# Kernel tuning notes

Hardware: AMD Instinct MI355X
Metric: run time of the kernel (lower is better)

Reference implementation:

```python
import jax, jax.numpy as jnp
import numpy as np

EMBED_DIM = 584  # module-global, used as softmax scale base (C ** -0.5)


def setup_inputs() -> dict:
    key = jax.random.key(0)
    ks = jax.random.split(key, 7)
    B, T, C, H, D = 16, 1024, 584, 8, 73
    x = jax.random.normal(ks[0], (B, T, C), dtype=jnp.float32)
    memory = jax.random.normal(ks[1], (B, T, C), dtype=jnp.float32)
    s = 0.02
    Wq = jax.random.normal(ks[2], (H, C, D), dtype=jnp.float32) * s
    Wk = jax.random.normal(ks[3], (H, C, D), dtype=jnp.float32) * s
    Wv = jax.random.normal(ks[4], (H, C, D), dtype=jnp.float32) * s
    Wp = jax.random.normal(ks[5], (C, C), dtype=jnp.float32) * s
    bp = jnp.zeros((C,), dtype=jnp.float32)
    return {"x": x, "memory": memory, "Wq": Wq, "Wk": Wk, "Wv": Wv, "Wp": Wp, "bp": bp}


def reference(x, memory, Wq, Wk, Wv, Wp, bp):
    B, T, C = x.shape
    # per-head projections, vectorized over heads: [B, H, T, D]
    q = jnp.einsum('btc,hcd->bhtd', x, Wq)
    k = jnp.einsum('bsc,hcd->bhsd', memory, Wk)
    v = jnp.einsum('btc,hcd->bhtd', x, Wv)  # NOTE: value from x, per original code
    # scale uses full embed dim C (not head size), per original code
    scores = jnp.einsum('bhtd,bhsd->bhts', q, k) * (C ** -0.5)
    weights = jax.nn.softmax(scores, axis=-1)
    # dropout is identity in eval/reference mode
    out = jnp.einsum('bhts,bhsd->bhtd', weights, v)  # requires S == T (matches original)
    out = out.transpose(0, 2, 1, 3).reshape(B, T, C)  # concat heads on last dim
    out = out @ Wp + bp  # output projection (dropout identity)
    return out
```

## Files before the change

### kernel.cpp

```cpp
#include <hip/hip_runtime.h>
#include <hip/hip_bf16.h>

typedef unsigned short u16;
typedef __attribute__((ext_vector_type(4))) unsigned short u16x4;
typedef __attribute__((ext_vector_type(8))) unsigned short u16x8;
typedef __attribute__((ext_vector_type(8))) __bf16 bf16x8;
typedef __attribute__((ext_vector_type(4))) float f32x4;

#define BB 16
#define TSEQ 1024
#define CC 584
#define HH 8
#define DHD 73
#define NR (BB*TSEQ)
#define KPW 608
#define KIT 19
#define DP 96
#define HD (HH*DP)
#define NP3 640
#define PPITCH 88
#define CEXP 0.0596985934f

__device__ __forceinline__ u16 f2bf(float f) {
  __bf16 h = (__bf16)f;
  return __builtin_bit_cast(u16, h);
}
__device__ __forceinline__ bf16x8 as_bf(u16x8 v) { return __builtin_bit_cast(bf16x8, v); }

#define GLL16(g, l) __builtin_amdgcn_global_load_lds( \
    (const __attribute__((address_space(1))) void*)(g), \
    (__attribute__((address_space(3))) void*)(l), 16, 0, 0)

#define PKA 9728
#define PKB 5472
#define PKC 1520
__global__ void pack_all_kernel(const float* __restrict__ x, const float* __restrict__ mem,
                                const float* __restrict__ Wq, const float* __restrict__ Wk,
                                const float* __restrict__ Wv, const float* __restrict__ Wp,
                                u16* __restrict__ xmb, u16* __restrict__ wt,
                                u16* __restrict__ wpt) {
  const int bidx = blockIdx.x;
  const int tid = threadIdx.x;
  if (bidx < PKA) {
    int idx = bidx * 256 + tid;
    int row = idx / (KPW / 8);
    int c8  = (idx % (KPW / 8)) * 8;
    u16x8 o = {0, 0, 0, 0, 0, 0, 0, 0};
    if (c8 < CC) {
      const float* src = (row < NR) ? &x[(size_t)row * CC + c8]
                                    : &mem[(size_t)(row - NR) * CC + c8];
      f32x4 a = *(const f32x4*)src;
      f32x4 b = *(const f32x4*)(src + 4);
#pragma unroll
      for (int t = 0; t < 4; t++) { o[t] = f2bf(a[t]); o[4 + t] = f2bf(b[t]); }
    }
    *(u16x8*)&xmb[(size_t)row * KPW + c8] = o;
  } else if (bidx < PKA + PKB) {
    int idx = (bidx - PKA) * 256 + tid;
    int w   = idx / (HD * KPW);
    int rem = idx % (HD * KPW);
    int n = rem / KPW;
    int k = rem % KPW;
    int h = n / DP, d = n % DP;
    u16 val = 0;
    if (d < DHD && k < CC) {
      const float* W = (w == 0) ? Wq : ((w == 1) ? Wv : Wk);
      val = f2bf(W[((size_t)h * CC + k) * DHD + d]);
    }
    wt[idx] = val;
  } else {
    int idx = (bidx - PKA - PKB) * 256 + tid;
    int n = idx / KPW;
    int c = idx % KPW;
    u16 val = 0;
    if (n < CC && c < CC) val = f2bf(Wp[(size_t)c * CC + n]);
    wpt[idx] = val;
  }
}

template <int MODE>
__global__ __launch_bounds__(256) void gemm_bt_kernel(
    const u16* __restrict__ A, const u16* __restrict__ Bt,
    void* __restrict__ CoutV, void* __restrict__ CoutV2,
    const float* __restrict__ bias) {
  const int mx = blockIdx.x;
  const bool isMem = (MODE == 4) && (mx >= 128);
  if (MODE == 4 && isMem && blockIdx.y >= 6) return;
  const int m0 = mx * 128;
  const int n0 = (MODE == 4) ? ((isMem ? 1536 : 0) + blockIdx.y * 128)
                             : blockIdx.y * 128;

  __shared__ u16 As[128 * 32];
  __shared__ u16 Bs[128 * 32];
  const int tid  = threadIdx.x;
  const int lane = tid & 63;
  const int wave = tid >> 6;
  const int wm = (wave >> 1) * 64;
  const int wn = (wave & 1) * 64;
  const int q15  = lane & 15;
  const int quad = lane >> 4;

  f32x4 acc[4][4];
#pragma unroll
  for (int i = 0; i < 4; i++)
#pragma unroll
    for (int j = 0; j < 4; j++) acc[i][j] = (f32x4){0.f, 0.f, 0.f, 0.f};

  const int r0 = tid >> 2;
  const int c0 = (tid & 3) * 8;
  u16* asd0 = &As[wave * 512];
  u16* asd1 = &As[2048 + wave * 512];
  u16* bsd0 = &Bs[wave * 512];
  u16* bsd1 = &Bs[2048 + wave * 512];
  const u16* gA0 = &A[(size_t)(m0 + r0) * KPW + c0];
  const u16* gA1 = gA0 + (size_t)64 * KPW;
  const u16* gB0 = &Bt[(size_t)(n0 + r0) * KPW + c0];
  const u16* gB1 = gB0 + (size_t)64 * KPW;

  for (int kk = 0; kk < KIT; ++kk) {
    GLL16(gA0, asd0);
    GLL16(gA1, asd1);
    GLL16(gB0, bsd0);
    GLL16(gB1, bsd1);
    gA0 += 32; gA1 += 32; gB0 += 32; gB1 += 32;
    __syncthreads();
    bf16x8 af[4], bfr[4];
#pragma unroll
    for (int i = 0; i < 4; i++)
      af[i] = as_bf(*(const u16x8*)&As[(wm + i * 16 + q15) * 32 + quad * 8]);
#pragma unroll
    for (int j = 0; j < 4; j++)
      bfr[j] = as_bf(*(const u16x8*)&Bs[(wn + j * 16 + q15) * 32 + quad * 8]);
#pragma unroll
    for (int i = 0; i < 4; i++)
#pragma unroll
      for (int j = 0; j < 4; j++)
        acc[i][j] = __builtin_amdgcn_mfma_f32_16x16x32_bf16(af[i], bfr[j], acc[i][j], 0, 0, 0);
    __syncthreads();
  }

#pragma unroll
  for (int i = 0; i < 4; i++) {
#pragma unroll
    for (int j = 0; j < 4; j++) {
      const int row = m0 + wm + i * 16 + quad * 4;
      const int col = n0 + wn + j * 16 + q15;
      if (MODE == 4) {
        if (isMem) {
          u16* Cout = (u16*)CoutV2;
          const int rk = row - NR;
          const int ck = col - 1536;
#pragma unroll
          for (int r = 0; r < 4; r++)
            Cout[(size_t)(rk + r) * HD + ck] = f2bf(acc[i][j][r]);
        } else if (col < HD) {
          u16* Cout = (u16*)CoutV;
#pragma unroll
          for (int r = 0; r < 4; r++)
            Cout[(size_t)(row + r) * HD + col] = f2bf(acc[i][j][r]);
        } else {
          u16* Cout = (u16*)CoutV;
          const int vn = col - HD;
          const int b  = row >> 10;
          const int tl = row & 1023;
          u16x4 pk;
#pragma unroll
          for (int r = 0; r < 4; r++) pk[r] = f2bf(acc[i][j][r]);
          *(u16x4*)&Cout[(size_t)(NR * HD) + ((size_t)(b * HD + vn)) * TSEQ + tl] = pk;
        }
      } else {
        if (col < CC) {
          float* Cout = (float*)CoutV;
          const float bv = bias[col];
#pragma unroll
          for (int r = 0; r < 4; r++)
            Cout[(size_t)(row + r) * CC + col] = acc[i][j][r] + bv;
        }
      }
    }
  }
}

__global__ __launch_bounds__(256, 3) void attn_kernel(
    const u16* __restrict__ qb, const u16* __restrict__ kb,
    const u16* __restrict__ vt, u16* __restrict__ attn) {
  __shared__ u16 smem[128 * 96 + 64 * 104 + 96 * 72];
  u16* Qs = smem;
  u16* Ks = smem + 128 * 96;
  u16* Vs = smem + 128 * 96 + 64 * 104;
  u16* Pt = smem;

  const int tid  = threadIdx.x;
  const int lane = tid & 63;
  const int wave = tid >> 6;
  const int q15  = lane & 15;
  const int quad = lane >> 4;
  const int bid  = blockIdx.x;
  const int loc  = bid >> 3;
  const int pair = (bid & 7) * 16 + (loc >> 3);
  const int b  = pair >> 3;
  const int h  = pair & 7;
  const int t0 = (loc & 7) * 128;
  const int wq0 = wave * 32;

  int krow[3], kc[3], vrow[3], vc[3];
#pragma unroll
  for (int p = 0; p < 3; p++) {
    int qk = tid + 256 * p;
    krow[p] = qk / 12; kc[p] = (qk % 12) * 8;
    int qv = tid + 256 * p;
    vrow[p] = qv / 8;  vc[p] = (qv % 8) * 8;
  }
  const u16* kbase = &kb[(size_t)(b * TSEQ) * HD + h * DP];
  const u16* vbase = &vt[(size_t)(b * HD + h * DP) * TSEQ];

  for (int q = tid; q < 128 * 12; q += 256) {
    int row = q / 12, c8 = (q % 12) * 8;
    *(u16x8*)&Qs[row * 96 + c8] =
        *(const u16x8*)&qb[(size_t)(b * TSEQ + t0 + row) * HD + h * DP + c8];
  }
  if (tid < 128) {
    const u16x8 z = {0, 0, 0, 0, 0, 0, 0, 0};
    size_t base = (size_t)(b * TSEQ + t0 + tid) * KPW + CC;
    *(u16x8*)&attn[base] = z;
    *(u16x8*)&attn[base + 8] = z;
    *(u16x8*)&attn[base + 16] = z;
  }
  __syncthreads();

  bf16x8 aq[2][3];
#pragma unroll
  for (int n = 0; n < 2; n++)
#pragma unroll
    for (int kcx = 0; kcx < 3; kcx++)
      aq[n][kcx] = as_bf(*(const u16x8*)&Qs[(wq0 + n * 16 + q15) * 96 + kcx * 32 + quad * 8]);

  float lsum[2] = {0.f, 0.f};
  f32x4 oacc[2][6];
#pragma unroll
  for (int m = 0; m < 2; m++)
#pragma unroll
    for (int jd = 0; jd < 6; jd++) oacc[m][jd] = (f32x4){0.f, 0.f, 0.f, 0.f};

  u16* Ptw = &Pt[wave * 32 * PPITCH];

  u16x8 kreg[3], vreg[3];
#pragma unroll
  for (int p = 0; p < 3; p++) {
    kreg[p] = *(const u16x8*)&kbase[(size_t)krow[p] * HD + kc[p]];
    vreg[p] = *(const u16x8*)&vbase[(size_t)vrow[p] * TSEQ + vc[p]];
  }

  for (int si = 0; si < 16; ++si) {
#pragma unroll
    for (int p = 0; p < 3; p++) {
      *(u16x8*)&Ks[krow[p] * 104 + kc[p]] = kreg[p];
      *(u16x8*)&Vs[vrow[p] * 72 + vc[p]]  = vreg[p];
    }
    __syncthreads();

    if (si < 15) {
      const int s1 = (si + 1) * 64;
#pragma unroll
      for (int p = 0; p < 3; p++) {
        kreg[p] = *(const u16x8*)&kbase[(size_t)(s1 + krow[p]) * HD + kc[p]];
        vreg[p] = *(const u16x8*)&vbase[(size_t)vrow[p] * TSEQ + s1 + vc[p]];
      }
    }

    f32x4 st[4][2];
#pragma unroll
    for (int mt = 0; mt < 4; mt++)
#pragma unroll
      for (int n = 0; n < 2; n++) st[mt][n] = (f32x4){0.f, 0.f, 0.f, 0.f};
#pragma unroll
    for (int kcx = 0; kcx < 3; kcx++) {
      bf16x8 ak[4];
#pragma unroll
      for (int mt = 0; mt < 4; mt++)
        ak[mt] = as_bf(*(const u16x8*)&Ks[(mt * 16 + q15) * 104 + kcx * 32 + quad * 8]);
#pragma unroll
      for (int mt = 0; mt < 4; mt++)
#pragma unroll
        for (int n = 0; n < 2; n++)
          st[mt][n] = __builtin_amdgcn_mfma_f32_16x16x32_bf16(ak[mt], aq[n][kcx], st[mt][n], 0, 0, 0);
    }

#pragma unroll
    for (int mt = 0; mt < 4; mt++)
#pragma unroll
      for (int n = 0; n < 2; n++) {
        f32x4 pv;
#pragma unroll
        for (int r = 0; r < 4; r++) pv[r] = __builtin_amdgcn_exp2f(st[mt][n][r] * CEXP);
        lsum[n] += (pv[0] + pv[1]) + (pv[2] + pv[3]);
        u16x4 pk;
#pragma unroll
        for (int r = 0; r < 4; r++) pk[r] = f2bf(pv[r]);
        *(u16x4*)&Ptw[(n * 16 + q15) * PPITCH + mt * 16 + quad * 4] = pk;
      }

#pragma unroll
    for (int kcx = 0; kcx < 2; kcx++) {
      bf16x8 ap[2];
#pragma unroll
      for (int m = 0; m < 2; m++)
        ap[m] = as_bf(*(const u16x8*)&Ptw[(m * 16 + q15) * PPITCH + kcx * 32 + quad * 8]);
#pragma unroll
      for (int jd = 0; jd < 6; jd++) {
        bf16x8 bv = as_bf(*(const u16x8*)&Vs[(jd * 16 + q15) * 72 + kcx * 32 + quad * 8]);
#pragma unroll
        for (int m = 0; m < 2; m++)
          oacc[m][jd] = __builtin_amdgcn_mfma_f32_16x16x32_bf16(ap[m], bv, oacc[m][jd], 0, 0, 0);
      }
    }
    __syncthreads();
  }

  float lr[2];
#pragma unroll
  for (int n = 0; n < 2; n++) {
    float s = lsum[n];
    s += __shfl_xor(s, 16);
    s += __shfl_xor(s, 32);
    lr[n] = s;
  }

#pragma unroll
  for (int m = 0; m < 2; m++) {
#pragma unroll
    for (int r = 0; r < 4; r++) {
      const float inv = 1.f / __shfl(lr[m], quad * 4 + r);
      const int trow = t0 + wq0 + m * 16 + quad * 4 + r;
#pragma unroll
      for (int jd = 0; jd < 5; jd++) {
        const int d = jd * 16 + q15;
        if (d < DHD)
          attn[(size_t)(b * TSEQ + trow) * KPW + h * DHD + d] = f2bf(oacc[m][jd][r] * inv);
      }
    }
  }
}


extern "C" void kernel_launch(void* const* d_in, const int* in_sizes, int n_in,
                              void* d_out, int out_size, void* d_ws, size_t ws_size,
                              hipStream_t stream) {
  const float* x   = (const float*)d_in[0];
  const float* mem = (const float*)d_in[1];
  const float* Wq  = (const float*)d_in[2];
  const float* Wk  = (const float*)d_in[3];
  const float* Wv  = (const float*)d_in[4];
  const float* Wp  = (const float*)d_in[5];
  const float* bp  = (const float*)d_in[6];
  float* out = (float*)d_out;

  char* ws = (char*)d_ws;
  const size_t SZ_XMB = (size_t)2 * NR * KPW * 2;
  const size_t SZ_WT  = (size_t)3 * HD * KPW * 2;
  const size_t SZ_WPT = (size_t)NP3 * KPW * 2;
  const size_t SZ_QB  = (size_t)NR * HD * 2;

  u16* xmb    = (u16*)(ws);
  u16* attn_o = (u16*)(ws);
  u16* wt     = (u16*)(ws + SZ_XMB);
  u16* wp_t   = (u16*)(ws + SZ_XMB + SZ_WT);
  u16* q_buf  = (u16*)(ws + SZ_XMB + SZ_WT + SZ_WPT);
  u16* vt_buf = q_buf + (size_t)NR * HD;
  u16* k_buf  = (u16*)(ws + SZ_XMB + SZ_WT + SZ_WPT + 2 * SZ_QB);

  (void)in_sizes; (void)n_in; (void)out_size; (void)ws_size;

  pack_all_kernel<<<PKA + PKB + PKC, 256, 0, stream>>>(x, mem, Wq, Wk, Wv, Wp,
                                                       xmb, wt, wp_t);

  dim3 gproj(256, 12);
  gemm_bt_kernel<4><<<gproj, 256, 0, stream>>>(xmb, wt, q_buf, k_buf, nullptr);

  attn_kernel<<<BB * HH * (TSEQ / 128), 256, 0, stream>>>(q_buf, k_buf, vt_buf, attn_o);

  dim3 g3(NR / 128, NP3 / 128);
  gemm_bt_kernel<2><<<g3, 256, 0, stream>>>(attn_o, wp_t, out, nullptr, bp);
}
```

Baseline: 296.2 us.

## Replace projection GEMMs with 256x256-tile, 8-wave, double-buffered swizzled-LDS kernel

Both projection GEMMs are replaced by a 512-thread kernel that computes 256x256 output tiles with BK=64. It double-buffers global-to-LDS loads with XOR-swizzled layout and interleaves explicit barriers and waitcnts so loads overlap MFMA work. Blocks are remapped across XCDs. K padding grows from 608 to 640 and the output-projection N padding from 640 to 768, which adds some wasted compute and larger pack buffers. The kernel uses 128KB of dynamic LDS, which caps occupancy.

```diff
diff --git a/kernel.cpp b/kernel.cpp
--- a/kernel.cpp
+++ b/kernel.cpp
@@ -13,11 +13,10 @@
 #define HH 8
 #define DHD 73
 #define NR (BB*TSEQ)
-#define KPW 608
-#define KIT 19
+#define KPW 640
 #define DP 96
 #define HD (HH*DP)
-#define NP3 640
+#define NP3 768
 #define PPITCH 88
 #define CEXP 0.0596985934f
 
@@ -31,9 +30,14 @@
     (const __attribute__((address_space(1))) void*)(g), \
     (__attribute__((address_space(3))) void*)(l), 16, 0, 0)
 
-#define PKA 9728
-#define PKB 5472
-#define PKC 1520
+#define BARRIER() asm volatile("s_barrier" ::: "memory")
+#define LGKM0()   asm volatile("s_waitcnt lgkmcnt(0)" ::: "memory")
+#define VMW4()    asm volatile("s_waitcnt vmcnt(4)" ::: "memory")
+#define VMW0()    asm volatile("s_waitcnt vmcnt(0)" ::: "memory")
+
+#define PKA 10240
+#define PKB 5760
+#define PKC 1920
 __global__ void pack_all_kernel(const float* __restrict__ x, const float* __restrict__ mem,
                                 const float* __restrict__ Wq, const float* __restrict__ Wk,
                                 const float* __restrict__ Wv, const float* __restrict__ Wp,
@@ -78,106 +82,217 @@
   }
 }
 
+
+template <int B, int MH>
+__device__ __forceinline__ void lda_f(bf16x8 (&av)[4][2], const u16* lds,
+                                      int aRow, int sw0, int sw1) {
+#pragma unroll
+  for (int mq = 0; mq < 4; mq++) {
+    const int r = aRow + B * 16384 + MH * 4096 + mq * 1024;
+    av[mq][0] = as_bf(*(const u16x8*)&lds[r + sw0]);
+    av[mq][1] = as_bf(*(const u16x8*)&lds[r + sw1]);
+  }
+}
+template <int B, int NH>
+__device__ __forceinline__ void ldb_f(bf16x8 (&bv)[2][2], const u16* lds,
+                                      int bRow, int sw0, int sw1) {
+#pragma unroll
+  for (int nq = 0; nq < 2; nq++) {
+    const int r = 32768 + bRow + B * 16384 + NH * 2048 + nq * 1024;
+    bv[nq][0] = as_bf(*(const u16x8*)&lds[r + sw0]);
+    bv[nq][1] = as_bf(*(const u16x8*)&lds[r + sw1]);
+  }
+}
+template <int OP, int U>
+__device__ __forceinline__ void stg_f(const u16* g0, u16* l0, int t) {
+  GLL16(g0 + (size_t)(U * 64) * KPW + (size_t)t * 64,
+        l0 + OP * 32768 + (t & 1) * 16384 + U * 4096);
+}
+template <int MH, int NH>
+__device__ __forceinline__ void mm_f(f32x4 (&acc)[8][4], const bf16x8 (&av)[4][2],
+                                     const bf16x8 (&bv)[2][2]) {
+  __builtin_amdgcn_s_setprio(1);
+#pragma unroll
+  for (int mq = 0; mq < 4; mq++)
+#pragma unroll
+    for (int nq = 0; nq < 2; nq++) {
+      f32x4 c = acc[MH * 4 + mq][NH * 2 + nq];
+      c = __builtin_amdgcn_mfma_f32_16x16x32_bf16(av[mq][0], bv[nq][0], c, 0, 0, 0);
+      c = __builtin_amdgcn_mfma_f32_16x16x32_bf16(av[mq][1], bv[nq][1], c, 0, 0, 0);
+      acc[MH * 4 + mq][NH * 2 + nq] = c;
+    }
+  __builtin_amdgcn_s_setprio(0);
+}
+
 template <int MODE>
-__global__ __launch_bounds__(256) void gemm_bt_kernel(
+__global__ __launch_bounds__(512, 2) void gemm8_kernel(
     const u16* __restrict__ A, const u16* __restrict__ Bt,
     void* __restrict__ CoutV, void* __restrict__ CoutV2,
     const float* __restrict__ bias) {
-  const int mx = blockIdx.x;
-  const bool isMem = (MODE == 4) && (mx >= 128);
-  if (MODE == 4 && isMem && blockIdx.y >= 6) return;
-  const int m0 = mx * 128;
-  const int n0 = (MODE == 4) ? ((isMem ? 1536 : 0) + blockIdx.y * 128)
-                             : blockIdx.y * 128;
-
-  __shared__ u16 As[128 * 32];
-  __shared__ u16 Bs[128 * 32];
+  extern __shared__ u16 lds[];
   const int tid  = threadIdx.x;
   const int lane = tid & 63;
-  const int wave = tid >> 6;
-  const int wm = (wave >> 1) * 64;
-  const int wn = (wave & 1) * 64;
   const int q15  = lane & 15;
   const int quad = lane >> 4;
-
-  f32x4 acc[4][4];
-#pragma unroll
-  for (int i = 0; i < 4; i++)
+  const int wave = tid >> 6;
+  const int wmi  = wave >> 2;
+  const int wni  = wave & 3;
+
+  const int cpx = gridDim.x >> 3;
+  const int bid = (blockIdx.x & 7) * cpx + (blockIdx.x >> 3);
+
+  int m0, n0, npart;
+  if (MODE == 4) {
+    if (bid < 384) {
+      m0 = (bid / 6) * 256; int nt = bid % 6;
+      n0 = nt * 256; npart = (nt >= 3) ? 1 : 0;
+    } else {
+      int b2 = bid - 384;
+      m0 = NR + (b2 / 3) * 256; n0 = 1536 + (b2 % 3) * 256; npart = 2;
+    }
+  } else {
+    m0 = (bid / 3) * 256; n0 = (bid % 3) * 256; npart = 0;
+  }
+
+  const int tr   = tid >> 3;
+  const int scol = ((tid & 7) ^ (tr & 7)) * 8;
+  const u16* gA = &A[(size_t)(m0 + tr) * KPW + scol];
+  const u16* gB = &Bt[(size_t)(n0 + tr) * KPW + scol];
+  u16* ldst = &lds[tid * 8];
+
+  const int rb  = q15 & 7;
+  const int sw0 = (quad ^ rb) * 8;
+  const int sw1 = ((quad + 4) ^ rb) * 8;
+  const int aRow = (wmi * 128 + q15) * 64;
+  const int bRow = (wni * 64 + q15) * 64;
+
+  f32x4 acc[8][4];
+#pragma unroll
+  for (int i = 0; i < 8; i++)
 #pragma unroll
     for (int j = 0; j < 4; j++) acc[i][j] = (f32x4){0.f, 0.f, 0.f, 0.f};
-
-  const int r0 = tid >> 2;
-  const int c0 = (tid & 3) * 8;
-  u16* asd0 = &As[wave * 512];
-  u16* asd1 = &As[2048 + wave * 512];
-  u16* bsd0 = &Bs[wave * 512];
-  u16* bsd1 = &Bs[2048 + wave * 512];
-  const u16* gA0 = &A[(size_t)(m0 + r0) * KPW + c0];
-  const u16* gA1 = gA0 + (size_t)64 * KPW;
-  const u16* gB0 = &Bt[(size_t)(n0 + r0) * KPW + c0];
-  const u16* gB1 = gB0 + (size_t)64 * KPW;
-
-  for (int kk = 0; kk < KIT; ++kk) {
-    GLL16(gA0, asd0);
-    GLL16(gA1, asd1);
-    GLL16(gB0, bsd0);
-    GLL16(gB1, bsd1);
-    gA0 += 32; gA1 += 32; gB0 += 32; gB1 += 32;
-    __syncthreads();
-    bf16x8 af[4], bfr[4];
-#pragma unroll
-    for (int i = 0; i < 4; i++)
-      af[i] = as_bf(*(const u16x8*)&As[(wm + i * 16 + q15) * 32 + quad * 8]);
-#pragma unroll
-    for (int j = 0; j < 4; j++)
-      bfr[j] = as_bf(*(const u16x8*)&Bs[(wn + j * 16 + q15) * 32 + quad * 8]);
-#pragma unroll
-    for (int i = 0; i < 4; i++)
-#pragma unroll
-      for (int j = 0; j < 4; j++)
-        acc[i][j] = __builtin_amdgcn_mfma_f32_16x16x32_bf16(af[i], bfr[j], acc[i][j], 0, 0, 0);
-    __syncthreads();
-  }
-
-#pragma unroll
-  for (int i = 0; i < 4; i++) {
-#pragma unroll
-    for (int j = 0; j < 4; j++) {
-      const int row = m0 + wm + i * 16 + quad * 4;
-      const int col = n0 + wn + j * 16 + q15;
-      if (MODE == 4) {
-        if (isMem) {
-          u16* Cout = (u16*)CoutV2;
-          const int rk = row - NR;
-          const int ck = col - 1536;
+  bf16x8 av[4][2], bv[2][2];
+
+  stg_f<0,0>(gA, ldst, 0); stg_f<0,1>(gA, ldst, 0);
+  stg_f<0,2>(gA, ldst, 0); stg_f<0,3>(gA, ldst, 0);
+  stg_f<1,0>(gB, ldst, 0); stg_f<1,1>(gB, ldst, 0);
+  stg_f<1,2>(gB, ldst, 0); stg_f<1,3>(gB, ldst, 0);
+  stg_f<0,0>(gA, ldst, 1); stg_f<0,2>(gA, ldst, 1);
+  stg_f<0,1>(gA, ldst, 1); stg_f<0,3>(gA, ldst, 1);
+  VMW4(); BARRIER();
+
+#pragma unroll 1
+  for (int i = 0; i < 5; ++i) {
+    const int t1 = 2 * i + 1;
+    const int t2 = 2 * i + 2;
+    const bool st = (i < 4);
+    lda_f<0,0>(av, lds, aRow, sw0, sw1);
+    ldb_f<0,0>(bv, lds, bRow, sw0, sw1);
+    stg_f<1,0>(gB, ldst, t1); stg_f<1,1>(gB, ldst, t1);
+    stg_f<1,2>(gB, ldst, t1); stg_f<1,3>(gB, ldst, t1);
+    BARRIER(); LGKM0();
+    mm_f<0,0>(acc, av, bv);
+    BARRIER();
+    ldb_f<0,1>(bv, lds, bRow, sw0, sw1);
+    if (st) { stg_f<0,0>(gA, ldst, t2); stg_f<0,2>(gA, ldst, t2); }
+    BARRIER(); LGKM0();
+    mm_f<0,1>(acc, av, bv);
+    BARRIER();
+    lda_f<0,1>(av, lds, aRow, sw0, sw1);
+    ldb_f<0,0>(bv, lds, bRow, sw0, sw1);
+    BARRIER(); LGKM0();
+    mm_f<1,0>(acc, av, bv);
+    BARRIER();
+    ldb_f<0,1>(bv, lds, bRow, sw0, sw1);
+    if (st) { stg_f<0,1>(gA, ldst, t2); stg_f<0,3>(gA, ldst, t2); }
+    BARRIER(); LGKM0();
+    mm_f<1,1>(acc, av, bv);
+    if (st) { VMW4(); } else { VMW0(); }
+    BARRIER();
+    lda_f<1,0>(av, lds, aRow, sw0, sw1);
+    ldb_f<1,0>(bv, lds, bRow, sw0, sw1);
+    if (st) { stg_f<1,0>(gB, ldst, t2); stg_f<1,1>(gB, ldst, t2); }
+    BARRIER(); LGKM0();
+    mm_f<0,0>(acc, av, bv);
+    BARRIER();
+    ldb_f<1,1>(bv, lds, bRow, sw0, sw1);
+    if (st) { stg_f<1,2>(gB, ldst, t2); stg_f<1,3>(gB, ldst, t2); }
+    BARRIER(); LGKM0();
+    mm_f<0,1>(acc, av, bv);
+    BARRIER();
+    lda_f<1,1>(av, lds, aRow, sw0, sw1);
+    ldb_f<1,0>(bv, lds, bRow, sw0, sw1);
+    if (st) { stg_f<0,0>(gA, ldst, t1 + 2); stg_f<0,2>(gA, ldst, t1 + 2); }
+    BARRIER(); LGKM0();
+    mm_f<1,0>(acc, av, bv);
+    BARRIER();
+    ldb_f<1,1>(bv, lds, bRow, sw0, sw1);
+    if (st) { stg_f<0,1>(gA, ldst, t1 + 2); stg_f<0,3>(gA, ldst, t1 + 2); }
+    BARRIER(); LGKM0();
+    mm_f<1,1>(acc, av, bv);
+    if (st) { VMW4(); }
+    BARRIER();
+  }
+
+  const int rowb = m0 + wmi * 128 + quad * 4;
+  const int colb = n0 + wni * 64 + q15;
+  if (MODE == 4) {
+    if (npart == 2) {
+      u16* Cout = (u16*)CoutV2;
+#pragma unroll
+      for (int mf = 0; mf < 8; mf++)
+#pragma unroll
+        for (int nf = 0; nf < 4; nf++) {
+          const int rk = rowb + mf * 16 - NR;
+          const int ck = colb + nf * 16 - 1536;
 #pragma unroll
           for (int r = 0; r < 4; r++)
-            Cout[(size_t)(rk + r) * HD + ck] = f2bf(acc[i][j][r]);
-        } else if (col < HD) {
-          u16* Cout = (u16*)CoutV;
+            Cout[(size_t)(rk + r) * HD + ck] = f2bf(acc[mf][nf][r]);
+        }
+    } else if (npart == 0) {
+      u16* Cout = (u16*)CoutV;
+#pragma unroll
+      for (int mf = 0; mf < 8; mf++)
+#pragma unroll
+        for (int nf = 0; nf < 4; nf++) {
+          const int row = rowb + mf * 16;
+          const int col = colb + nf * 16;
 #pragma unroll
           for (int r = 0; r < 4; r++)
-            Cout[(size_t)(row + r) * HD + col] = f2bf(acc[i][j][r]);
-        } else {
-          u16* Cout = (u16*)CoutV;
-          const int vn = col - HD;
-          const int b  = row >> 10;
-          const int tl = row & 1023;
+            Cout[(size_t)(row + r) * HD + col] = f2bf(acc[mf][nf][r]);
+        }
+    } else {
+      u16* Cout = (u16*)CoutV;
+#pragma unroll
+      for (int mf = 0; mf < 8; mf++) {
+        const int row = rowb + mf * 16;
+        const int bb  = row >> 10;
+        const int tl  = row & 1023;
+#pragma unroll
+        for (int nf = 0; nf < 4; nf++) {
+          const int vn = colb + nf * 16 - HD;
           u16x4 pk;
 #pragma unroll
-          for (int r = 0; r < 4; r++) pk[r] = f2bf(acc[i][j][r]);
-          *(u16x4*)&Cout[(size_t)(NR * HD) + ((size_t)(b * HD + vn)) * TSEQ + tl] = pk;
-        }
-      } else {
-        if (col < CC) {
-          float* Cout = (float*)CoutV;
-          const float bv = bias[col];
-#pragma unroll
-          for (int r = 0; r < 4; r++)
-            Cout[(size_t)(row + r) * CC + col] = acc[i][j][r] + bv;
+          for (int r = 0; r < 4; r++) pk[r] = f2bf(acc[mf][nf][r]);
+          *(u16x4*)&Cout[(size_t)(NR * HD) + ((size_t)(bb * HD + vn)) * TSEQ + tl] = pk;
         }
       }
     }
+  } else {
+    float* Cout = (float*)CoutV;
+#pragma unroll
+    for (int mf = 0; mf < 8; mf++)
+#pragma unroll
+      for (int nf = 0; nf < 4; nf++) {
+        const int col = colb + nf * 16;
+        if (col < CC) {
+          const float bvv = bias[col];
+          const int row = rowb + mf * 16;
+#pragma unroll
+          for (int r = 0; r < 4; r++)
+            Cout[(size_t)(row + r) * CC + col] = acc[mf][nf][r] + bvv;
+        }
+      }
   }
 }
 
@@ -222,9 +337,8 @@
   if (tid < 128) {
     const u16x8 z = {0, 0, 0, 0, 0, 0, 0, 0};
     size_t base = (size_t)(b * TSEQ + t0 + tid) * KPW + CC;
-    *(u16x8*)&attn[base] = z;
-    *(u16x8*)&attn[base + 8] = z;
-    *(u16x8*)&attn[base + 16] = z;
+#pragma unroll
+    for (int c = 0; c < (KPW - CC) / 8; c++) *(u16x8*)&attn[base + c * 8] = z;
   }
   __syncthreads();
 
@@ -371,14 +485,21 @@
 
   (void)in_sizes; (void)n_in; (void)out_size; (void)ws_size;
 
+  static bool s_attr = false;
+  if (!s_attr) {
+    (void)hipFuncSetAttribute((const void*)gemm8_kernel<4>,
+                              hipFuncAttributeMaxDynamicSharedMemorySize, 131072);
+    (void)hipFuncSetAttribute((const void*)gemm8_kernel<2>,
+                              hipFuncAttributeMaxDynamicSharedMemorySize, 131072);
+    s_attr = true;
+  }
+
   pack_all_kernel<<<PKA + PKB + PKC, 256, 0, stream>>>(x, mem, Wq, Wk, Wv, Wp,
                                                        xmb, wt, wp_t);
 
-  dim3 gproj(256, 12);
-  gemm_bt_kernel<4><<<gproj, 256, 0, stream>>>(xmb, wt, q_buf, k_buf, nullptr);
+  gemm8_kernel<4><<<576, 512, 131072, stream>>>(xmb, wt, q_buf, k_buf, nullptr);
 
   attn_kernel<<<BB * HH * (TSEQ / 128), 256, 0, stream>>>(q_buf, k_buf, vt_buf, attn_o);
 
-  dim3 g3(NR / 128, NP3 / 128);
-  gemm_bt_kernel<2><<<g3, 256, 0, stream>>>(attn_o, wp_t, out, nullptr, bp);
-}
+  gemm8_kernel<2><<<192, 512, 131072, stream>>>(attn_o, wp_t, out, nullptr, bp);
+}
```

After: 292.2 us. About the same (-1.3%).
